# Kernel optimization log

Measured on AMD Instinct MI355X. Metric: run time of the kernel, lower is better.

## Reference

```python
import jax, jax.numpy as jnp
import numpy as np

DECAY = 0.8
EPS = 1e-05
COMMIT_W = 0.25
N, D, K = 32768, 128, 4096


def setup_inputs() -> dict:
    key = jax.random.key(0)
    k1, k2, k3, k4 = jax.random.split(key, 4)
    x = jax.random.normal(k1, (N, D), dtype=jnp.float32)
    embed = jax.random.normal(k2, (1, K, D), dtype=jnp.float32)
    cluster_size = jax.random.uniform(k3, (1, K), dtype=jnp.float32)
    embed_avg = jax.random.normal(k4, (1, K, D), dtype=jnp.float32)
    return {"x": x, "embed": embed, "cluster_size": cluster_size, "embed_avg": embed_avg}


def reference(x, embed, cluster_size, embed_avg):
    # x: [n, d]; embed: [1, K, d] (num_codebooks = 1, squeezed as in batched_embedding)
    e = embed[0]                                   # [K, d]
    K_ = e.shape[0]
    # negative squared euclidean distance (== -cdist^2 ordering, same argmin as -cdist)
    x2 = jnp.sum(x * x, axis=-1, keepdims=True)    # [n, 1]
    e2 = jnp.sum(e * e, axis=-1)                   # [K]
    dist = -(x2 - 2.0 * (x @ e.T) + e2)            # [n, K]
    embed_ind = jnp.argmax(dist, axis=-1)          # [n] cluster assignment (argmin distance)
    # differentiable embedding lookup (one-hot @ embed == gather)
    quantize = jnp.take(e, embed_ind, axis=0)      # [n, d]
    # EMA codebook statistics (training-time buffer updates)
    ones = jnp.ones((x.shape[0],), dtype=x.dtype)
    bins = jax.ops.segment_sum(ones, embed_ind, num_segments=K_)         # [K] bincount
    embed_sum = jax.ops.segment_sum(x, embed_ind, num_segments=K_)       # [K, d] scatter-add
    cs_new = cluster_size[0] * DECAY + (1.0 - DECAY) * bins
    ea_new = embed_avg[0] * DECAY + (1.0 - DECAY) * embed_sum
    n_total = jnp.sum(cs_new)
    cluster = (cs_new + EPS) / (n_total + K_ * EPS) * n_total            # laplace smoothing
    embed_normalized = ea_new / cluster[:, None]                         # [K, d]
    # commitment loss: mse(quantize.detach(), x) * weight
    commit_loss = COMMIT_W * jnp.mean((jax.lax.stop_gradient(quantize) - x) ** 2)
    return (quantize, embed_ind, commit_loss, cs_new[None], embed_normalized[None])
```

## Files before the change

### kernel.cpp

```cpp
#include <hip/hip_runtime.h>

#define NROWS 32768
#define DIM   128
#define KCODES 4096
#define DECAYF 0.8f
#define EPSF 1e-5f
#define COMMITW 0.25f

typedef _Float16 half8 __attribute__((ext_vector_type(8)));
typedef _Float16 half2v __attribute__((ext_vector_type(2)));
typedef float float4v __attribute__((ext_vector_type(4)));

__global__ __launch_bounds__(256) void esplit_kernel(const float* __restrict__ embed,
                                                     _Float16* __restrict__ estg,
                                                     float* __restrict__ e2h,
                                                     int* __restrict__ bins,
                                                     float* __restrict__ loss) {
    int code = blockIdx.x * 4 + (threadIdx.x >> 6);
    int lane = threadIdx.x & 63;
    float2 v = ((const float2*)(embed + (size_t)code * DIM))[lane];
    float s = v.x * v.x + v.y * v.y;
    #pragma unroll
    for (int off = 32; off > 0; off >>= 1) s += __shfl_down(s, off, 64);
    if (lane == 0) e2h[code] = 0.5f * s;
    if (lane == 1) bins[code] = 0;
    if (code == 0 && lane == 2) *loss = 0.f;

    int d = lane * 2;
    int ks = d >> 5, q = (d >> 3) & 3, j = d & 7;
    _Float16 h0 = (_Float16)v.x, l0 = (_Float16)(v.x - (float)h0);
    _Float16 h1 = (_Float16)v.y, l1 = (_Float16)(v.y - (float)h1);
    int chunk = code >> 6, c6 = code & 63;
    size_t base = (size_t)chunk * 16384;
    size_t hidx = base + (size_t)(( 0 + ks * 4 + q) * 64 + c6) * 8 + j;
    size_t lidx = base + (size_t)((16 + ks * 4 + q) * 64 + c6) * 8 + j;
    *(half2v*)&estg[hidx] = (half2v){h0, h1};
    *(half2v*)&estg[lidx] = (half2v){l0, l1};
}

__global__ __launch_bounds__(512, 2) void argmax_kernel(const float* __restrict__ x,
                                                        const _Float16* __restrict__ estg,
                                                        const float* __restrict__ e2h,
                                                        int* __restrict__ ind,
                                                        float* __restrict__ out_ind,
                                                        int* __restrict__ bins,
                                                        float* __restrict__ loss) {
    __shared__ float rv[8][64];
    __shared__ int   ri[8][64];
    __shared__ float x2s[128];

    int tid = threadIdx.x;
    int lane = tid & 63;
    int w = tid >> 6;
    int j = w & 3;
    int rh = w >> 2;
    int m15 = lane & 15;
    int q = (lane >> 4) & 3;
    int n0 = blockIdx.x * 128;

    half8 Ah[4][4], Al[4][4];
    float xsq[4];
    #pragma unroll
    for (int rt = 0; rt < 4; ++rt) {
        xsq[rt] = 0.f;
        #pragma unroll
        for (int ks = 0; ks < 4; ++ks) {
            const float* p = x + (size_t)(n0 + rh * 64 + rt * 16 + m15) * DIM + ks * 32 + q * 8;
            float4 a = *(const float4*)p;
            float4 b = *(const float4*)(p + 4);
            float f[8] = {a.x, a.y, a.z, a.w, b.x, b.y, b.z, b.w};
            half8 H, L;
            #pragma unroll
            for (int e = 0; e < 8; ++e) {
                _Float16 h = (_Float16)f[e];
                H[e] = h;
                L[e] = (_Float16)(f[e] - (float)h);
                xsq[rt] += f[e] * f[e];
            }
            Ah[rt][ks] = H;
            Al[rt][ks] = L;
        }
        xsq[rt] += __shfl_xor(xsq[rt], 16, 64);
        xsq[rt] += __shfl_xor(xsq[rt], 32, 64);
    }
    if (j == 0 && lane < 16) {
        #pragma unroll
        for (int rt = 0; rt < 4; ++rt) x2s[rh * 64 + rt * 16 + m15] = xsq[rt];
    }

    float best[4][4];
    int   bidx[4][4];
    #pragma unroll
    for (int rt = 0; rt < 4; ++rt)
        #pragma unroll
        for (int r = 0; r < 4; ++r) { best[rt][r] = -3.0e38f; bidx[rt][r] = 0; }

    const _Float16* bbase = estg + (size_t)(j * 16 + m15) * 8 + (size_t)q * 512;
    const int cm = j * 16 + m15;

    half8 B0h[4], B0l[4], B1h[4], B1l[4];
    float e20, e21;

    {
        const _Float16* cb = bbase;
        #pragma unroll
        for (int ks = 0; ks < 4; ++ks) {
            B0h[ks] = *(const half8*)(cb + ks * 2048);
            B0l[ks] = *(const half8*)(cb + 8192 + ks * 2048);
        }
        e20 = e2h[cm];
    }

    #pragma unroll 1
    for (int ch = 0; ch < 64; ch += 2) {
        {
            const _Float16* cb = bbase + (size_t)(ch + 1) * 16384;
            #pragma unroll
            for (int ks = 0; ks < 4; ++ks) {
                B1h[ks] = *(const half8*)(cb + ks * 2048);
                B1l[ks] = *(const half8*)(cb + 8192 + ks * 2048);
            }
            e21 = e2h[(ch + 1) * 64 + cm];
        }
        {
            float4v acc[4];
            #pragma unroll
            for (int rt = 0; rt < 4; ++rt) acc[rt] = (float4v){-e20, -e20, -e20, -e20};
            __builtin_amdgcn_s_setprio(1);
            #pragma unroll
            for (int ks = 0; ks < 4; ++ks)
                #pragma unroll
                for (int rt = 0; rt < 4; ++rt) {
                    acc[rt] = __builtin_amdgcn_mfma_f32_16x16x32_f16(Ah[rt][ks], B0h[ks], acc[rt], 0, 0, 0);
                    acc[rt] = __builtin_amdgcn_mfma_f32_16x16x32_f16(Al[rt][ks], B0h[ks], acc[rt], 0, 0, 0);
                    acc[rt] = __builtin_amdgcn_mfma_f32_16x16x32_f16(Ah[rt][ks], B0l[ks], acc[rt], 0, 0, 0);
                }
            __builtin_amdgcn_s_setprio(0);
            int c = ch * 64 + cm;
            #pragma unroll
            for (int rt = 0; rt < 4; ++rt)
                #pragma unroll
                for (int r = 0; r < 4; ++r) {
                    float s = acc[rt][r];
                    if (s > best[rt][r]) { best[rt][r] = s; bidx[rt][r] = c; }
                }
        }
        if (ch + 2 < 64) {
            const _Float16* cb = bbase + (size_t)(ch + 2) * 16384;
            #pragma unroll
            for (int ks = 0; ks < 4; ++ks) {
                B0h[ks] = *(const half8*)(cb + ks * 2048);
                B0l[ks] = *(const half8*)(cb + 8192 + ks * 2048);
            }
            e20 = e2h[(ch + 2) * 64 + cm];
        }
        {
            float4v acc[4];
            #pragma unroll
            for (int rt = 0; rt < 4; ++rt) acc[rt] = (float4v){-e21, -e21, -e21, -e21};
            __builtin_amdgcn_s_setprio(1);
            #pragma unroll
            for (int ks = 0; ks < 4; ++ks)
                #pragma unroll
                for (int rt = 0; rt < 4; ++rt) {
                    acc[rt] = __builtin_amdgcn_mfma_f32_16x16x32_f16(Ah[rt][ks], B1h[ks], acc[rt], 0, 0, 0);
                    acc[rt] = __builtin_amdgcn_mfma_f32_16x16x32_f16(Al[rt][ks], B1h[ks], acc[rt], 0, 0, 0);
                    acc[rt] = __builtin_amdgcn_mfma_f32_16x16x32_f16(Ah[rt][ks], B1l[ks], acc[rt], 0, 0, 0);
                }
            __builtin_amdgcn_s_setprio(0);
            int c = (ch + 1) * 64 + cm;
            #pragma unroll
            for (int rt = 0; rt < 4; ++rt)
                #pragma unroll
                for (int r = 0; r < 4; ++r) {
                    float s = acc[rt][r];
                    if (s > best[rt][r]) { best[rt][r] = s; bidx[rt][r] = c; }
                }
        }
    }

    #pragma unroll
    for (int rt = 0; rt < 4; ++rt)
        #pragma unroll
        for (int r = 0; r < 4; ++r) {
            float bv = best[rt][r];
            int   bi = bidx[rt][r];
            #pragma unroll
            for (int m = 1; m <= 8; m <<= 1) {
                float ov = __shfl_xor(bv, m, 64);
                int   oi = __shfl_xor(bi, m, 64);
                if (ov > bv || (ov == bv && oi < bi)) { bv = ov; bi = oi; }
            }
            if (m15 == 0) {
                int rl = rt * 16 + q * 4 + r;
                rv[w][rl] = bv;
                ri[w][rl] = bi;
            }
        }
    __syncthreads();
    if (tid < 128) {
        int rhh = tid >> 6;
        int rl  = tid & 63;
        float bv = rv[rhh * 4][rl];
        int   bi = ri[rhh * 4][rl];
        #pragma unroll
        for (int jj = 1; jj < 4; ++jj) {
            float ov = rv[rhh * 4 + jj][rl];
            int   oi = ri[rhh * 4 + jj][rl];
            if (ov > bv || (ov == bv && oi < bi)) { bv = ov; bi = oi; }
        }
        ind[n0 + tid] = bi;
        out_ind[n0 + tid] = (float)bi;
        atomicAdd(&bins[bi], 1);
        float lp = x2s[tid] - 2.0f * bv;
        #pragma unroll
        for (int off = 32; off > 0; off >>= 1) lp += __shfl_down(lp, off, 64);
        if ((tid & 63) == 0) atomicAdd(loss, lp);
    }
}

__global__ __launch_bounds__(1024) void scan_kernel(const int* __restrict__ bins,
                                                    const float* __restrict__ cluster_size,
                                                    const float* __restrict__ loss,
                                                    int* __restrict__ offsets,
                                                    int* __restrict__ cursor,
                                                    float* __restrict__ out_cs,
                                                    float* __restrict__ ntot,
                                                    float* __restrict__ out_loss) {
    __shared__ int   wtot[16];
    __shared__ float fred[16];
    int t = threadIdx.x;
    int lane = t & 63, wv = t >> 6;
    int b[4];
    float cs[4];
    float csum = 0.f;
    int s = 0;
    #pragma unroll
    for (int e = 0; e < 4; ++e) {
        b[e] = bins[t * 4 + e];
        s += b[e];
        cs[e] = cluster_size[t * 4 + e] * DECAYF + (1.0f - DECAYF) * (float)b[e];
        csum += cs[e];
    }
    int sc = s;
    #pragma unroll
    for (int off = 1; off < 64; off <<= 1) {
        int v = __shfl_up(sc, off, 64);
        if (lane >= off) sc += v;
    }
    float fc = csum;
    #pragma unroll
    for (int off = 32; off > 0; off >>= 1) fc += __shfl_down(fc, off, 64);
    if (lane == 63) wtot[wv] = sc;
    if (lane == 0) fred[wv] = fc;
    __syncthreads();
    if (t < 16) {
        int v = wtot[t];
        int scv = v;
        #pragma unroll
        for (int off = 1; off < 16; off <<= 1) {
            int u = __shfl_up(scv, off, 64);
            if (t >= off) scv += u;
        }
        wtot[t] = scv - v;
    }
    if (t == 0) {
        float tot = 0.f;
        #pragma unroll
        for (int i = 0; i < 16; ++i) tot += fred[i];
        *ntot = tot;
        *out_loss = COMMITW * (*loss) / (float)((size_t)NROWS * DIM);
    }
    __syncthreads();
    int ex = sc - s + wtot[wv];
    #pragma unroll
    for (int e = 0; e < 4; ++e) {
        offsets[t * 4 + e] = ex;
        cursor[t * 4 + e] = ex;
        out_cs[t * 4 + e] = cs[e];
        ex += b[e];
    }
}

__global__ __launch_bounds__(256) void reorder_kernel(const int* __restrict__ ind,
                                                      int* __restrict__ cursor,
                                                      int* __restrict__ rowids,
                                                      int* __restrict__ codesorted,
                                                      const float* __restrict__ embed,
                                                      float* __restrict__ out_q,
                                                      float* __restrict__ esum) {
    int tid = threadIdx.x;
    int lane = tid & 63;
    int wv = blockIdx.x * 4 + (tid >> 6);

    esum[blockIdx.x * 256 + tid] = 0.f;

    if (lane < 4) {
        int row = wv * 4 + lane;
        int k = ind[row];
        int pos = atomicAdd(&cursor[k], 1);
        rowids[pos] = row;
        codesorted[pos] = k;
    }
    #pragma unroll
    for (int i = 0; i < 4; ++i) {
        int row = wv * 4 + i;
        int k = ind[row];
        float2 qv = ((const float2*)(embed + (size_t)k * DIM))[lane];
        ((float2*)(out_q + (size_t)row * DIM))[lane] = qv;
    }
}

#define WROWS 16
__global__ __launch_bounds__(256) void segred_kernel(const float* __restrict__ x,
                                                     const int* __restrict__ rowids,
                                                     const int* __restrict__ codesorted,
                                                     const int* __restrict__ offsets,
                                                     const int* __restrict__ bins,
                                                     float* __restrict__ esum) {
    int tid = threadIdx.x;
    int lane = tid & 63;
    int wv = blockIdx.x * 4 + (tid >> 6);
    int w0 = wv * WROWS;

    int i16 = lane & (WROWS - 1);
    int rowv = rowids[w0 + i16];
    int kv   = codesorted[w0 + i16];

    float2 xv[WROWS];
    #pragma unroll
    for (int i = 0; i < WROWS; ++i) {
        int row = __shfl(rowv, i, 64);
        xv[i] = ((const float2*)(x + (size_t)row * DIM))[lane];
    }

    int curk = __shfl(kv, 0, 64);
    float2 acc = {0.f, 0.f};

    #pragma unroll
    for (int i = 0; i < WROWS; ++i) {
        int k = __shfl(kv, i, 64);
        if (k != curk) {
            int sbeg = offsets[curk];
            int send = sbeg + bins[curk];
            float* ep = esum + (size_t)curk * DIM + lane * 2;
            if (sbeg >= w0 && send <= w0 + WROWS) {
                *(float2*)ep = acc;
            } else {
                atomicAdd(ep, acc.x);
                atomicAdd(ep + 1, acc.y);
            }
            curk = k;
            acc = (float2){0.f, 0.f};
        }
        acc.x += xv[i].x;
        acc.y += xv[i].y;
    }
    {
        int sbeg = offsets[curk];
        int send = sbeg + bins[curk];
        float* ep = esum + (size_t)curk * DIM + lane * 2;
        if (sbeg >= w0 && send <= w0 + WROWS) {
            *(float2*)ep = acc;
        } else {
            atomicAdd(ep, acc.x);
            atomicAdd(ep + 1, acc.y);
        }
    }
}

__global__ __launch_bounds__(256) void norm_kernel(const float* __restrict__ esum,
                                                   const float* __restrict__ embed_avg,
                                                   const float* __restrict__ out_cs,
                                                   const float* __restrict__ ntot,
                                                   float* __restrict__ out_norm) {
    int idx = blockIdx.x * 256 + threadIdx.x;
    int k = idx >> 6;
    float nt = *ntot;
    float cs = out_cs[k];
    float cluster = (cs + EPSF) / (nt + (float)KCODES * EPSF) * nt;
    float inv = 1.0f / cluster;
    float2 es = ((const float2*)esum)[idx];
    float2 ea = ((const float2*)embed_avg)[idx];
    float2 o;
    o.x = (ea.x * DECAYF + (1.0f - DECAYF) * es.x) * inv;
    o.y = (ea.y * DECAYF + (1.0f - DECAYF) * es.y) * inv;
    ((float2*)out_norm)[idx] = o;
}

extern "C" void kernel_launch(void* const* d_in, const int* in_sizes, int n_in,
                              void* d_out, int out_size, void* d_ws, size_t ws_size,
                              hipStream_t stream) {
    const float* x            = (const float*)d_in[0];
    const float* embed        = (const float*)d_in[1];
    const float* cluster_size = (const float*)d_in[2];
    const float* embed_avg    = (const float*)d_in[3];

    float* out      = (float*)d_out;
    float* out_q    = out;
    float* out_ind  = out + 4194304;
    float* out_loss = out_ind + 32768;
    float* out_cs   = out_loss + 1;
    float* out_norm = out_cs + 4096;

    char* ws = (char*)d_ws;
    _Float16* estg = (_Float16*)ws;
    float* e2h   = (float*)(ws + 2097152);
    int*   ind   = (int*)(ws + 2113536);
    int*   offsets = (int*)(ws + 2244608);
    int*   cursor  = (int*)(ws + 2260992);
    int*   rowids  = (int*)(ws + 2277376);
    int*   codesorted = (int*)(ws + 2408448);
    float* loss  = (float*)(ws + 2539520);
    float* ntot  = loss + 1;
    int*   bins  = (int*)(ws + 2539776);
    float* esum  = (float*)(ws + 2556160);

    esplit_kernel<<<KCODES / 4, 256, 0, stream>>>(embed, estg, e2h, bins, loss);
    argmax_kernel<<<NROWS / 128, 512, 0, stream>>>(x, estg, e2h, ind, out_ind,
                                                   bins, loss);
    scan_kernel<<<1, 1024, 0, stream>>>(bins, cluster_size, loss, offsets, cursor,
                                        out_cs, ntot, out_loss);
    reorder_kernel<<<NROWS / 16, 256, 0, stream>>>(ind, cursor, rowids, codesorted,
                                                   embed, out_q, esum);
    segred_kernel<<<NROWS / WROWS / 4, 256, 0, stream>>>(x, rowids, codesorted,
                                                         offsets, bins, esum);
    norm_kernel<<<KCODES * DIM / 2 / 256, 256, 0, stream>>>(esum, embed_avg, out_cs,
                                                            ntot, out_norm);
}
```

Measured before the change: 194.7 us.

## Fuse gather and scatter-add into argmax kernel, drop sort-based segment reduction

The argmax kernel now keeps each row's chosen code in shared memory. It then writes the quantized rows and scatter-adds x into esum directly with float atomics, replacing the scan, reorder and segmented-reduce kernels. esum zeroing moves into the codebook-split kernel, and the scan kernel is reduced to a stats-only kernel. This removes two launches, the ind/rowids/codesorted round trips and the counting-sort pass. The cost is 4M per-element global atomics with possible contention on popular codes, and a float summation order that is no longer deterministic.

```diff
diff --git a/kernel.cpp b/kernel.cpp
--- a/kernel.cpp
+++ b/kernel.cpp
@@ -15,9 +15,13 @@
                                                      _Float16* __restrict__ estg,
                                                      float* __restrict__ e2h,
                                                      int* __restrict__ bins,
-                                                     float* __restrict__ loss) {
+                                                     float* __restrict__ loss,
+                                                     float* __restrict__ esum) {
     int code = blockIdx.x * 4 + (threadIdx.x >> 6);
     int lane = threadIdx.x & 63;
+
+    ((float2*)esum)[blockIdx.x * 256 + threadIdx.x] = (float2){0.f, 0.f};
+
     float2 v = ((const float2*)(embed + (size_t)code * DIM))[lane];
     float s = v.x * v.x + v.y * v.y;
     #pragma unroll
@@ -41,13 +45,16 @@
 __global__ __launch_bounds__(512, 2) void argmax_kernel(const float* __restrict__ x,
                                                         const _Float16* __restrict__ estg,
                                                         const float* __restrict__ e2h,
-                                                        int* __restrict__ ind,
                                                         float* __restrict__ out_ind,
                                                         int* __restrict__ bins,
-                                                        float* __restrict__ loss) {
+                                                        float* __restrict__ loss,
+                                                        const float* __restrict__ embed,
+                                                        float* __restrict__ out_q,
+                                                        float* __restrict__ esum) {
     __shared__ float rv[8][64];
     __shared__ int   ri[8][64];
     __shared__ float x2s[128];
+    __shared__ int   kk[128];
 
     int tid = threadIdx.x;
     int lane = tid & 63;
@@ -209,7 +216,7 @@
             int   oi = ri[rhh * 4 + jj][rl];
             if (ov > bv || (ov == bv && oi < bi)) { bv = ov; bi = oi; }
         }
-        ind[n0 + tid] = bi;
+        kk[tid] = bi;
         out_ind[n0 + tid] = (float)bi;
         atomicAdd(&bins[bi], 1);
         float lp = x2s[tid] - 2.0f * bv;
@@ -217,155 +224,50 @@
         for (int off = 32; off > 0; off >>= 1) lp += __shfl_down(lp, off, 64);
         if ((tid & 63) == 0) atomicAdd(loss, lp);
     }
-}
-
-__global__ __launch_bounds__(1024) void scan_kernel(const int* __restrict__ bins,
-                                                    const float* __restrict__ cluster_size,
-                                                    const float* __restrict__ loss,
-                                                    int* __restrict__ offsets,
-                                                    int* __restrict__ cursor,
-                                                    float* __restrict__ out_cs,
-                                                    float* __restrict__ ntot,
-                                                    float* __restrict__ out_loss) {
-    __shared__ int   wtot[16];
+    __syncthreads();
+
+    {
+        int rb = w * 16;
+        #pragma unroll 4
+        for (int i = 0; i < 16; ++i) {
+            int row = rb + i;
+            int k = kk[row];
+            float2 xv = ((const float2*)(x + (size_t)(n0 + row) * DIM))[lane];
+            float2 qv = ((const float2*)(embed + (size_t)k * DIM))[lane];
+            ((float2*)(out_q + (size_t)(n0 + row) * DIM))[lane] = qv;
+            float* ep = esum + (size_t)k * DIM + lane * 2;
+            atomicAdd(ep, xv.x);
+            atomicAdd(ep + 1, xv.y);
+        }
+    }
+}
+
+__global__ __launch_bounds__(1024) void stats_kernel(const int* __restrict__ bins,
+                                                     const float* __restrict__ cluster_size,
+                                                     const float* __restrict__ loss,
+                                                     float* __restrict__ out_cs,
+                                                     float* __restrict__ ntot,
+                                                     float* __restrict__ out_loss) {
     __shared__ float fred[16];
     int t = threadIdx.x;
     int lane = t & 63, wv = t >> 6;
-    int b[4];
-    float cs[4];
     float csum = 0.f;
-    int s = 0;
     #pragma unroll
     for (int e = 0; e < 4; ++e) {
-        b[e] = bins[t * 4 + e];
-        s += b[e];
-        cs[e] = cluster_size[t * 4 + e] * DECAYF + (1.0f - DECAYF) * (float)b[e];
-        csum += cs[e];
-    }
-    int sc = s;
-    #pragma unroll
-    for (int off = 1; off < 64; off <<= 1) {
-        int v = __shfl_up(sc, off, 64);
-        if (lane >= off) sc += v;
-    }
-    float fc = csum;
-    #pragma unroll
-    for (int off = 32; off > 0; off >>= 1) fc += __shfl_down(fc, off, 64);
-    if (lane == 63) wtot[wv] = sc;
-    if (lane == 0) fred[wv] = fc;
+        float cs = cluster_size[t * 4 + e] * DECAYF + (1.0f - DECAYF) * (float)bins[t * 4 + e];
+        out_cs[t * 4 + e] = cs;
+        csum += cs;
+    }
+    #pragma unroll
+    for (int off = 32; off > 0; off >>= 1) csum += __shfl_down(csum, off, 64);
+    if (lane == 0) fred[wv] = csum;
     __syncthreads();
-    if (t < 16) {
-        int v = wtot[t];
-        int scv = v;
-        #pragma unroll
-        for (int off = 1; off < 16; off <<= 1) {
-            int u = __shfl_up(scv, off, 64);
-            if (t >= off) scv += u;
-        }
-        wtot[t] = scv - v;
-    }
     if (t == 0) {
         float tot = 0.f;
         #pragma unroll
         for (int i = 0; i < 16; ++i) tot += fred[i];
         *ntot = tot;
         *out_loss = COMMITW * (*loss) / (float)((size_t)NROWS * DIM);
-    }
-    __syncthreads();
-    int ex = sc - s + wtot[wv];
-    #pragma unroll
-    for (int e = 0; e < 4; ++e) {
-        offsets[t * 4 + e] = ex;
-        cursor[t * 4 + e] = ex;
-        out_cs[t * 4 + e] = cs[e];
-        ex += b[e];
-    }
-}
-
-__global__ __launch_bounds__(256) void reorder_kernel(const int* __restrict__ ind,
-                                                      int* __restrict__ cursor,
-                                                      int* __restrict__ rowids,
-                                                      int* __restrict__ codesorted,
-                                                      const float* __restrict__ embed,
-                                                      float* __restrict__ out_q,
-                                                      float* __restrict__ esum) {
-    int tid = threadIdx.x;
-    int lane = tid & 63;
-    int wv = blockIdx.x * 4 + (tid >> 6);
-
-    esum[blockIdx.x * 256 + tid] = 0.f;
-
-    if (lane < 4) {
-        int row = wv * 4 + lane;
-        int k = ind[row];
-        int pos = atomicAdd(&cursor[k], 1);
-        rowids[pos] = row;
-        codesorted[pos] = k;
-    }
-    #pragma unroll
-    for (int i = 0; i < 4; ++i) {
-        int row = wv * 4 + i;
-        int k = ind[row];
-        float2 qv = ((const float2*)(embed + (size_t)k * DIM))[lane];
-        ((float2*)(out_q + (size_t)row * DIM))[lane] = qv;
-    }
-}
-
-#define WROWS 16
-__global__ __launch_bounds__(256) void segred_kernel(const float* __restrict__ x,
-                                                     const int* __restrict__ rowids,
-                                                     const int* __restrict__ codesorted,
-                                                     const int* __restrict__ offsets,
-                                                     const int* __restrict__ bins,
-                                                     float* __restrict__ esum) {
-    int tid = threadIdx.x;
-    int lane = tid & 63;
-    int wv = blockIdx.x * 4 + (tid >> 6);
-    int w0 = wv * WROWS;
-
-    int i16 = lane & (WROWS - 1);
-    int rowv = rowids[w0 + i16];
-    int kv   = codesorted[w0 + i16];
-
-    float2 xv[WROWS];
-    #pragma unroll
-    for (int i = 0; i < WROWS; ++i) {
-        int row = __shfl(rowv, i, 64);
-        xv[i] = ((const float2*)(x + (size_t)row * DIM))[lane];
-    }
-
-    int curk = __shfl(kv, 0, 64);
-    float2 acc = {0.f, 0.f};
-
-    #pragma unroll
-    for (int i = 0; i < WROWS; ++i) {
-        int k = __shfl(kv, i, 64);
-        if (k != curk) {
-            int sbeg = offsets[curk];
-            int send = sbeg + bins[curk];
-            float* ep = esum + (size_t)curk * DIM + lane * 2;
-            if (sbeg >= w0 && send <= w0 + WROWS) {
-                *(float2*)ep = acc;
-            } else {
-                atomicAdd(ep, acc.x);
-                atomicAdd(ep + 1, acc.y);
-            }
-            curk = k;
-            acc = (float2){0.f, 0.f};
-        }
-        acc.x += xv[i].x;
-        acc.y += xv[i].y;
-    }
-    {
-        int sbeg = offsets[curk];
-        int send = sbeg + bins[curk];
-        float* ep = esum + (size_t)curk * DIM + lane * 2;
-        if (sbeg >= w0 && send <= w0 + WROWS) {
-            *(float2*)ep = acc;
-        } else {
-            atomicAdd(ep, acc.x);
-            atomicAdd(ep + 1, acc.y);
-        }
     }
 }
 
@@ -406,25 +308,16 @@
     char* ws = (char*)d_ws;
     _Float16* estg = (_Float16*)ws;
     float* e2h   = (float*)(ws + 2097152);
-    int*   ind   = (int*)(ws + 2113536);
-    int*   offsets = (int*)(ws + 2244608);
-    int*   cursor  = (int*)(ws + 2260992);
-    int*   rowids  = (int*)(ws + 2277376);
-    int*   codesorted = (int*)(ws + 2408448);
-    float* loss  = (float*)(ws + 2539520);
+    float* loss  = (float*)(ws + 2113536);
     float* ntot  = loss + 1;
-    int*   bins  = (int*)(ws + 2539776);
-    float* esum  = (float*)(ws + 2556160);
-
-    esplit_kernel<<<KCODES / 4, 256, 0, stream>>>(embed, estg, e2h, bins, loss);
-    argmax_kernel<<<NROWS / 128, 512, 0, stream>>>(x, estg, e2h, ind, out_ind,
-                                                   bins, loss);
-    scan_kernel<<<1, 1024, 0, stream>>>(bins, cluster_size, loss, offsets, cursor,
-                                        out_cs, ntot, out_loss);
-    reorder_kernel<<<NROWS / 16, 256, 0, stream>>>(ind, cursor, rowids, codesorted,
+    int*   bins  = (int*)(ws + 2113792);
+    float* esum  = (float*)(ws + 2130176);
+
+    esplit_kernel<<<KCODES / 4, 256, 0, stream>>>(embed, estg, e2h, bins, loss, esum);
+    argmax_kernel<<<NROWS / 128, 512, 0, stream>>>(x, estg, e2h, out_ind, bins, loss,
                                                    embed, out_q, esum);
-    segred_kernel<<<NROWS / WROWS / 4, 256, 0, stream>>>(x, rowids, codesorted,
-                                                         offsets, bins, esum);
+    stats_kernel<<<1, 1024, 0, stream>>>(bins, cluster_size, loss, out_cs, ntot,
+                                         out_loss);
     norm_kernel<<<KCODES * DIM / 2 / 256, 256, 0, stream>>>(esum, embed_avg, out_cs,
                                                             ntot, out_norm);
 }
```

New measurement: 230.2 us. +18.2%, slower.
